# Optimization experiments

Hardware: AMD Instinct MI355X
Metric: run time of the kernel (lower is better)

The kernel has to match this reference:

```python
import jax, jax.numpy as jnp
import numpy as np

# ---- config (mirrors the torch forward's scalar args) ----
NCONF, NATOMS = 1024, 64
NOShfS, NOShfR, NOShfTheta, NOShfA = 16, 16, 16, 16
OEtaS, OEtaR, OEtaA, OZeta = 16.0, 8.0, 8.0, 8.0
L_S, U_S = -4.0, 4.0
L_R, U_R = 0.0, 4.0
L_A, U_A = 0.0, 4.0
L_T, U_T = 0.0, float(np.pi)
NAOV = 4          # p-orbital atomic-orbital vectors
NS = 9            # s coefficients
# upper-triangular pair indices (i<j) in the same row-major order as the torch double loop
_IU, _JU = np.triu_indices(NAOV, k=1)   # 6 pairs


def setup_inputs() -> dict:
    key = jax.random.key(0)
    k1, k2, k3 = jax.random.split(key, 3)
    coefficients = jax.random.normal(k1, (NCONF, NATOMS, 21), dtype=jnp.float32)
    normalization_library = jax.random.normal(k2, (7, 21), dtype=jnp.float32)
    species = jax.random.randint(k3, (NCONF, NATOMS), 0, 7, dtype=jnp.int64)
    return {"coefficients": coefficients,
            "normalization_library": normalization_library,
            "species": species}


def _forward(coefficients):
    nconf, natoms, _ = coefficients.shape
    dt = coefficients.dtype
    s_coeffs = coefficients[..., :NS]                               # [c,n,9]
    p_matrix = coefficients[..., NS:NS + 3 * NAOV].reshape(nconf, natoms, NAOV, 3)

    # --- s-coefficient Gaussian expansion ---
    OShfS = jnp.linspace(L_S, U_S, NOShfS, dtype=dt)                # [S]
    s_aev = jnp.exp(-OEtaS * (s_coeffs[..., None] - OShfS) ** 2)    # [c,n,9,S]
    s_aev = s_aev.reshape(nconf, natoms, NS * NOShfS)

    # --- radial expansion of p-vector norms ---
    p_norms = jnp.linalg.norm(p_matrix, axis=-1)                    # [c,n,4]
    OShfR = jnp.linspace(L_R, U_R, NOShfR, dtype=dt)
    radial_aev = jnp.exp(-OEtaR * (p_norms[..., None] - OShfR) ** 2)
    radial_aev = radial_aev.reshape(nconf, natoms, NAOV * NOShfR)

    # --- pairwise angles between the 4 p-vectors (6 pairs) ---
    zero_mask = jnp.all(jnp.abs(p_matrix) < 1e-12, axis=-1)         # [c,n,4]
    p_hat = jnp.where(zero_mask[..., None], 0.0,
                      p_matrix / p_norms[..., None])
    cos_all = jnp.einsum('cnid,cnjd->cnij', p_hat, p_hat)           # [c,n,4,4]
    cos_pairs = jnp.clip(cos_all[..., _IU, _JU], -0.9999, 0.9999)   # [c,n,6]
    angles = jnp.arccos(cos_pairs)
    avdist = (p_norms[..., _IU] + p_norms[..., _JU]) * 0.5          # [c,n,6]

    # --- angular expansion with radial coupling ---
    OShfTheta = jnp.linspace(L_T, U_T, NOShfTheta, dtype=dt)
    f_theta = (2.0 ** (1.0 - OZeta)) * \
        ((1.0 + jnp.cos(angles[..., None] - OShfTheta)) * 0.5) ** OZeta  # [c,n,6,T]
    OShfA = jnp.linspace(L_A, U_A, NOShfA, dtype=dt)
    f_dist = jnp.exp(-OEtaA * (avdist[..., None] - OShfA) ** 2)          # [c,n,6,A]
    # outer product over (theta, avdist) grids -> [c,n,6,T,A]
    angular_aev = (f_theta[..., :, None] * f_dist[..., None, :])
    angular_aev = angular_aev.reshape(nconf, natoms, angles.shape[-1] * NOShfTheta * NOShfA)

    return jnp.concatenate((s_aev, radial_aev, angular_aev), axis=-1)


def reference(coefficients, normalization_library, species):
    # normalization_library and species are unused on this code path
    # (basis='sp', use_simple_orbital_aev=False), matching the torch source.
    return _forward(coefficients)
```

## Files before the change

### kernel.cpp

```cpp
#include <hip/hip_runtime.h>


namespace {

typedef float f4 __attribute__((ext_vector_type(4)));

constexpr int kPerAtom = 1744;
constexpr int kQ = kPerAtom / 4;
constexpr float kPi = 3.14159265358979323846f;

__global__ __launch_bounds__(448) void aev_kernel(
    const float* __restrict__ coeff, float* __restrict__ out)
{
    __shared__ float sCC[6], sSN[6], sAV[6];
    __shared__ float sFT[96];
    __shared__ float sFD[96];

    const int atom = blockIdx.x;
    const float* __restrict__ c = coeff + (long long)atom * 21;
    const int q = threadIdx.x;

    if (q < 6) {
        const int p = q;
        const int i = (p < 3) ? 0 : ((p < 5) ? 1 : 2);
        const int j = (p < 3) ? (p + 1) : ((p < 5) ? (p - 1) : 3);
        const float ax = c[9 + 3 * i], ay = c[10 + 3 * i], az = c[11 + 3 * i];
        const float bx = c[9 + 3 * j], by = c[10 + 3 * j], bz = c[11 + 3 * j];
        const float na2 = ax * ax + ay * ay + az * az;
        const float nb2 = bx * bx + by * by + bz * bz;
        const float dot = ax * bx + ay * by + az * bz;
        const float ia = (na2 > 1e-24f) ? __builtin_amdgcn_rsqf(na2) : 0.0f;
        const float ib = (nb2 > 1e-24f) ? __builtin_amdgcn_rsqf(nb2) : 0.0f;
        float cc = dot * ia * ib;
        cc = fminf(0.9999f, fmaxf(-0.9999f, cc));
        sCC[p] = cc;
        sSN[p] = __builtin_amdgcn_sqrtf(1.0f - cc * cc);
        sAV[p] = 0.5f * (na2 * ia + nb2 * ib);
    }
    __syncthreads();

    if (q < 96) {
        const int p = q >> 4, t = q & 15;
        const float th = (float)t * (kPi / 15.0f);
        const float ct = __cosf(th), st = __sinf(th);
        const float x = 0.5f * (1.0f + sCC[p] * ct + sSN[p] * st);
        const float x2 = x * x, x4 = x2 * x2;
        sFT[q] = 0.0078125f * (x4 * x4);
    } else if (q < 192) {
        const int idx = q - 96;
        const int p = idx >> 4, a = idx & 15;
        const float d = sAV[p] - (float)a * (4.0f / 15.0f);
        sFD[idx] = __expf(-8.0f * d * d);
    }
    __syncthreads();

    float r[4];
    if (q < 36) {
        const int i  = q >> 2;
        const int k0 = (q & 3) << 2;
        const float s = c[i];
#pragma unroll
        for (int u = 0; u < 4; ++u) {
            const float d = s - (-4.0f + (float)(k0 + u) * (8.0f / 15.0f));
            r[u] = __expf(-16.0f * d * d);
        }
    } else if (q < 52) {
        const int i  = (q - 36) >> 2;
        const int k0 = ((q - 36) & 3) << 2;
        const float px = c[9 + 3 * i], py = c[10 + 3 * i], pz = c[11 + 3 * i];
        const float n = __builtin_amdgcn_sqrtf(px * px + py * py + pz * pz);
#pragma unroll
        for (int u = 0; u < 4; ++u) {
            const float d = n - (float)(k0 + u) * (4.0f / 15.0f);
            r[u] = __expf(-8.0f * d * d);
        }
    } else if (q < kQ) {
        const int e  = (q - 52) << 2;
        const int p  = e >> 8;
        const int tt = (e >> 4) & 15;
        const int a0 = e & 15;
        const float ft = sFT[p * 16 + tt];
        const f4 fd = *reinterpret_cast<const f4*>(&sFD[p * 16 + a0]);
#pragma unroll
        for (int u = 0; u < 4; ++u) r[u] = ft * fd[u];
    }

    if (q < kQ) {
        f4* __restrict__ outv = reinterpret_cast<f4*>(out + (long long)atom * kPerAtom);
        const f4 v = {r[0], r[1], r[2], r[3]};
        outv[q] = v;
    }
}

}

extern "C" void kernel_launch(void* const* d_in, const int* in_sizes, int n_in,
                              void* d_out, int out_size, void* d_ws, size_t ws_size,
                              hipStream_t stream) {
    const float* coeff = (const float*)d_in[0];
    float* out = (float*)d_out;
    aev_kernel<<<dim3(1024 * 64), dim3(448), 0, stream>>>(coeff, out);
}
```

Before: 514.8 us.

## Assign one wavefront per atom in a persistent grid-stride loop

Replaces the one-block-per-atom launch with a persistent grid of 2048 blocks of four waves, where each wave processes atoms in a grid-stride loop using a private LDS table. Block-wide __syncthreads are replaced by wave-local lgkmcnt waits, and the s and radial inputs are staged in LDS so all 64 lanes share the output writes across seven passes. The goal is to remove block launch and barrier overhead and the idle threads of the 448-thread blocks. The cost is less parallelism per atom and reliance on wave-synchronous LDS ordering without explicit barriers.

```diff
diff --git a/kernel.cpp b/kernel.cpp
--- a/kernel.cpp
+++ b/kernel.cpp
@@ -5,90 +5,110 @@
 
 typedef float f4 __attribute__((ext_vector_type(4)));
 
-constexpr int kPerAtom = 1744;
-constexpr int kQ = kPerAtom / 4;
+constexpr int kPerAtom  = 1744;
+constexpr int kQ        = kPerAtom / 4;
+constexpr int kAtoms    = 1024 * 64;
+constexpr int kBlocks   = 2048;
+constexpr int kWavesTot = kBlocks * 4;
 constexpr float kPi = 3.14159265358979323846f;
 
-__global__ __launch_bounds__(448) void aev_kernel(
+__device__ inline void wave_lds_fence() {
+    asm volatile("s_waitcnt lgkmcnt(0)" ::: "memory");
+}
+
+__global__ __launch_bounds__(256) void aev_kernel(
     const float* __restrict__ coeff, float* __restrict__ out)
 {
-    __shared__ float sCC[6], sSN[6], sAV[6];
-    __shared__ float sFT[96];
-    __shared__ float sFD[96];
+    __shared__ float tab[4][224];
 
-    const int atom = blockIdx.x;
-    const float* __restrict__ c = coeff + (long long)atom * 21;
-    const int q = threadIdx.x;
+    const int lane = threadIdx.x & 63;
+    const int wid  = (blockIdx.x << 2) | (threadIdx.x >> 6);
+    float* __restrict__ t = tab[threadIdx.x >> 6];
 
-    if (q < 6) {
-        const int p = q;
-        const int i = (p < 3) ? 0 : ((p < 5) ? 1 : 2);
-        const int j = (p < 3) ? (p + 1) : ((p < 5) ? (p - 1) : 3);
-        const float ax = c[9 + 3 * i], ay = c[10 + 3 * i], az = c[11 + 3 * i];
-        const float bx = c[9 + 3 * j], by = c[10 + 3 * j], bz = c[11 + 3 * j];
-        const float na2 = ax * ax + ay * ay + az * az;
-        const float nb2 = bx * bx + by * by + bz * bz;
-        const float dot = ax * bx + ay * by + az * bz;
-        const float ia = (na2 > 1e-24f) ? __builtin_amdgcn_rsqf(na2) : 0.0f;
-        const float ib = (nb2 > 1e-24f) ? __builtin_amdgcn_rsqf(nb2) : 0.0f;
-        float cc = dot * ia * ib;
-        cc = fminf(0.9999f, fmaxf(-0.9999f, cc));
-        sCC[p] = cc;
-        sSN[p] = __builtin_amdgcn_sqrtf(1.0f - cc * cc);
-        sAV[p] = 0.5f * (na2 * ia + nb2 * ib);
-    }
-    __syncthreads();
+    for (int atom = wid; atom < kAtoms; atom += kWavesTot) {
+        const float* __restrict__ ca = coeff + (long long)atom * 21;
 
-    if (q < 96) {
-        const int p = q >> 4, t = q & 15;
-        const float th = (float)t * (kPi / 15.0f);
-        const float ct = __cosf(th), st = __sinf(th);
-        const float x = 0.5f * (1.0f + sCC[p] * ct + sSN[p] * st);
-        const float x2 = x * x, x4 = x2 * x2;
-        sFT[q] = 0.0078125f * (x4 * x4);
-    } else if (q < 192) {
-        const int idx = q - 96;
-        const int p = idx >> 4, a = idx & 15;
-        const float d = sAV[p] - (float)a * (4.0f / 15.0f);
-        sFD[idx] = __expf(-8.0f * d * d);
-    }
-    __syncthreads();
+        if (lane < 6) {
+            const int p = lane;
+            const int i = (p < 3) ? 0 : ((p < 5) ? 1 : 2);
+            const int j = (p < 3) ? (p + 1) : ((p < 5) ? (p - 1) : 3);
+            const float ax = ca[9 + 3 * i], ay = ca[10 + 3 * i], az = ca[11 + 3 * i];
+            const float bx = ca[9 + 3 * j], by = ca[10 + 3 * j], bz = ca[11 + 3 * j];
+            const float na2 = ax * ax + ay * ay + az * az;
+            const float nb2 = bx * bx + by * by + bz * bz;
+            const float dot = ax * bx + ay * by + az * bz;
+            const float ia = (na2 > 1e-24f) ? __builtin_amdgcn_rsqf(na2) : 0.0f;
+            const float ib = (nb2 > 1e-24f) ? __builtin_amdgcn_rsqf(nb2) : 0.0f;
+            float cc = dot * ia * ib;
+            cc = fminf(0.9999f, fmaxf(-0.9999f, cc));
+            t[205 + p] = cc;
+            t[211 + p] = __builtin_amdgcn_sqrtf(1.0f - cc * cc);
+            t[217 + p] = 0.5f * (na2 * ia + nb2 * ib);
+        } else if (lane < 10) {
+            const int i = lane - 6;
+            const float px = ca[9 + 3 * i], py = ca[10 + 3 * i], pz = ca[11 + 3 * i];
+            t[201 + i] = __builtin_amdgcn_sqrtf(px * px + py * py + pz * pz);
+        } else if (lane < 19) {
+            t[192 + (lane - 10)] = ca[lane - 10];
+        }
+        wave_lds_fence();
 
-    float r[4];
-    if (q < 36) {
-        const int i  = q >> 2;
-        const int k0 = (q & 3) << 2;
-        const float s = c[i];
 #pragma unroll
-        for (int u = 0; u < 4; ++u) {
-            const float d = s - (-4.0f + (float)(k0 + u) * (8.0f / 15.0f));
-            r[u] = __expf(-16.0f * d * d);
+        for (int r = 0; r < 3; ++r) {
+            const int k = r * 64 + lane;
+            float v;
+            if (k < 96) {
+                const int p = k >> 4, tt = k & 15;
+                const float th = (float)tt * (kPi / 15.0f);
+                const float x = 0.5f * (1.0f + t[205 + p] * __cosf(th)
+                                             + t[211 + p] * __sinf(th));
+                const float x2 = x * x, x4 = x2 * x2;
+                v = 0.0078125f * (x4 * x4);
+            } else {
+                const int m = k - 96;
+                const int p = m >> 4, a = m & 15;
+                const float d = t[217 + p] - (float)a * (4.0f / 15.0f);
+                v = __expf(-8.0f * d * d);
+            }
+            t[k] = v;
         }
-    } else if (q < 52) {
-        const int i  = (q - 36) >> 2;
-        const int k0 = ((q - 36) & 3) << 2;
-        const float px = c[9 + 3 * i], py = c[10 + 3 * i], pz = c[11 + 3 * i];
-        const float n = __builtin_amdgcn_sqrtf(px * px + py * py + pz * pz);
+        wave_lds_fence();
+
+        f4* __restrict__ outv = reinterpret_cast<f4*>(out + (long long)atom * kPerAtom);
 #pragma unroll
-        for (int u = 0; u < 4; ++u) {
-            const float d = n - (float)(k0 + u) * (4.0f / 15.0f);
-            r[u] = __expf(-8.0f * d * d);
+        for (int r = 0; r < 7; ++r) {
+            const int f = r * 64 + lane;
+            if (f < kQ) {
+                float rv[4];
+                if (f < 36) {
+                    const int i = f >> 2, k0 = (f & 3) << 2;
+                    const float s = t[192 + i];
+#pragma unroll
+                    for (int u = 0; u < 4; ++u) {
+                        const float d = s - (-4.0f + (float)(k0 + u) * (8.0f / 15.0f));
+                        rv[u] = __expf(-16.0f * d * d);
+                    }
+                } else if (f < 52) {
+                    const int i = (f - 36) >> 2, k0 = ((f - 36) & 3) << 2;
+                    const float n = t[201 + i];
+#pragma unroll
+                    for (int u = 0; u < 4; ++u) {
+                        const float d = n - (float)(k0 + u) * (4.0f / 15.0f);
+                        rv[u] = __expf(-8.0f * d * d);
+                    }
+                } else {
+                    const int e = (f - 52) << 2;
+                    const int p = e >> 8, tt = (e >> 4) & 15, a0 = e & 15;
+                    const float ftv = t[p * 16 + tt];
+                    const f4 fdv = *reinterpret_cast<const f4*>(&t[96 + p * 16 + a0]);
+#pragma unroll
+                    for (int u = 0; u < 4; ++u) rv[u] = ftv * fdv[u];
+                }
+                const f4 v = {rv[0], rv[1], rv[2], rv[3]};
+                outv[f] = v;
+            }
         }
-    } else if (q < kQ) {
-        const int e  = (q - 52) << 2;
-        const int p  = e >> 8;
-        const int tt = (e >> 4) & 15;
-        const int a0 = e & 15;
-        const float ft = sFT[p * 16 + tt];
-        const f4 fd = *reinterpret_cast<const f4*>(&sFD[p * 16 + a0]);
-#pragma unroll
-        for (int u = 0; u < 4; ++u) r[u] = ft * fd[u];
-    }
-
-    if (q < kQ) {
-        f4* __restrict__ outv = reinterpret_cast<f4*>(out + (long long)atom * kPerAtom);
-        const f4 v = {r[0], r[1], r[2], r[3]};
-        outv[q] = v;
+        wave_lds_fence();
     }
 }
 
@@ -99,5 +119,5 @@
                               hipStream_t stream) {
     const float* coeff = (const float*)d_in[0];
     float* out = (float*)d_out;
-    aev_kernel<<<dim3(1024 * 64), dim3(448), 0, stream>>>(coeff, out);
+    aev_kernel<<<dim3(kBlocks), dim3(256), 0, stream>>>(coeff, out);
 }
```

Measured after the change: 460.5 us. -10.5%, faster.
